# Performance work log

Hardware: AMD Instinct MI355X
Metric: run time of the kernel (lower is better)

## Reference

```python
import jax, jax.numpy as jnp
import numpy as np

N, E, DIN, DOUT = 10000, 160000, 256, 256
NEG_SLOPE = 0.2
BN_EPS = 1e-5
DROP_P = 0.5


def setup_inputs() -> dict:
    key = jax.random.key(0)
    ks = jax.random.split(key, 12)
    s = 1.0 / np.sqrt(DIN)
    return {
        "x": jax.random.normal(ks[0], (N, DIN), jnp.float32),
        "edge_index": jax.random.randint(ks[1], (2, E), 0, N, jnp.int64),
        "Wl": jax.random.normal(ks[2], (DIN, DOUT), jnp.float32) * s,
        "bl": jax.random.normal(ks[3], (DOUT,), jnp.float32) * s,
        "Wr": jax.random.normal(ks[4], (DIN, DOUT), jnp.float32) * s,
        "br": jax.random.normal(ks[5], (DOUT,), jnp.float32) * s,
        "att": jax.random.normal(ks[6], (DOUT,), jnp.float32) * (1.0 / np.sqrt(DOUT)),
        "bias": jax.random.normal(ks[7], (DOUT,), jnp.float32) * 0.01,
        "gamma": jnp.ones((DOUT,), jnp.float32),
        "beta": jnp.zeros((DOUT,), jnp.float32),
        "dropout_u": jax.random.uniform(ks[8], (N, DOUT), jnp.float32),
    }


def reference(x, edge_index, Wl, bl, Wr, br, att, bias, gamma, beta, dropout_u):
    n = x.shape[0]
    # GATv2Conv (heads=1): separate source/target linear maps
    xl = x @ Wl + bl  # source features [N, DOUT]
    xr = x @ Wr + br  # target features [N, DOUT]
    # add self-loops (PyG default add_self_loops=True)
    loop = jnp.arange(n, dtype=edge_index.dtype)
    src = jnp.concatenate([edge_index[0], loop])  # [E+N]
    dst = jnp.concatenate([edge_index[1], loop])
    # GATv2 attention: e = att . LeakyReLU(xl_j + xr_i)
    h = jax.nn.leaky_relu(xl[src] + xr[dst], NEG_SLOPE)  # [E+N, DOUT]
    alpha = h @ att  # [E+N]
    # segment softmax over destination nodes
    amax = jax.ops.segment_max(alpha, dst, num_segments=n)
    alpha = jnp.exp(alpha - amax[dst])
    denom = jax.ops.segment_sum(alpha, dst, num_segments=n)
    alpha = alpha / denom[dst]
    # scatter-add aggregate of weighted source features
    out = jax.ops.segment_sum(xl[src] * alpha[:, None], dst, num_segments=n)
    out = out + bias
    # ReLU -> dropout(p=0.5, training) -> BatchNorm (training stats)
    out = jax.nn.relu(out)
    mask = (dropout_u >= DROP_P).astype(out.dtype) / (1.0 - DROP_P)
    out = out * mask
    mean = out.mean(axis=0)
    var = out.var(axis=0)  # biased, as BatchNorm uses for normalization
    out = gamma * (out - mean) * jax.lax.rsqrt(var + BN_EPS) + beta
    return out
```

## Files before the change

kernel.cpp:

```cpp
#include <hip/hip_runtime.h>
#include <hip/hip_bf16.h>
#include <math.h>

#define D 256
#define CAP 128
#define NEG_SLOPE 0.2f
#define BN_EPS 1e-5f
#define NBKT 64

typedef __attribute__((ext_vector_type(8))) short bf16x8;
typedef __attribute__((ext_vector_type(8))) unsigned short ushort8;
typedef __attribute__((ext_vector_type(4))) float f32x4;

__device__ inline unsigned short f2bf(float f) {
    union { float f; unsigned u; } v; v.f = f;
    unsigned u = v.u;
    unsigned r = u + 0x7FFFu + ((u >> 16) & 1u);
    return (unsigned short)(r >> 16);
}
__device__ inline float bf2f(unsigned short u) {
    union { unsigned u; float f; } v; v.u = ((unsigned)u) << 16; return v.f;
}

__device__ __forceinline__ void gload16(const void* g, void* l) {
    __builtin_amdgcn_global_load_lds(
        (const __attribute__((address_space(1))) unsigned int*)g,
        (__attribute__((address_space(3))) unsigned int*)l,
        16, 0, 0);
}

__global__ void prep_kernel(const float* __restrict__ X,
                            const float* __restrict__ Wl, const float* __restrict__ Wr,
                            int* __restrict__ zero_base, int nzero, int nzb,
                            unsigned short* __restrict__ Bt,
                            unsigned short* __restrict__ Xbf, int N) {
    int b = blockIdx.x;
    if (b < nzb) {
        int idx = b * 256 + threadIdx.x;
        if (idx < nzero) zero_base[idx] = 0;
    } else if (b < nzb + 512) {
        int n = b - nzb;
        int k = threadIdx.x;
        const float* W = (n < 256) ? Wl : Wr;
        int nn = n & 255;
        int ks = k ^ ((n & 7) << 3);
        Bt[(size_t)n * 256 + ks] = f2bf(W[(size_t)k * 256 + nn]);
    } else {
        int idx = (b - nzb - 512) * 256 + threadIdx.x;
        int row = idx >> 5;
        int k0 = (idx & 31) * 8;
        int ks = k0 ^ ((row & 7) << 3);
        ushort8 v = {0, 0, 0, 0, 0, 0, 0, 0};
        if (row < N) {
            const float* src = X + (size_t)row * 256 + k0;
            float4 f0 = *(const float4*)(src);
            float4 f1 = *(const float4*)(src + 4);
            v[0] = f2bf(f0.x); v[1] = f2bf(f0.y);
            v[2] = f2bf(f0.z); v[3] = f2bf(f0.w);
            v[4] = f2bf(f1.x); v[5] = f2bf(f1.y);
            v[6] = f2bf(f1.z); v[7] = f2bf(f1.w);
        }
        *(ushort8*)(Xbf + (size_t)row * 256 + ks) = v;
    }
}

__global__ __launch_bounds__(256) void gemm_scatter_kernel(
    const unsigned short* __restrict__ Xbf, const unsigned short* __restrict__ Bt,
    const float* __restrict__ bl, const float* __restrict__ br,
    const int* __restrict__ ei, int* __restrict__ counts, int* __restrict__ ssrc,
    unsigned short* __restrict__ xlbf, float* __restrict__ xr,
    int M, int E, int N, int ngemm)
{
    if ((int)blockIdx.x >= ngemm) {
        int e = (blockIdx.x - ngemm) * 256 + threadIdx.x;
        if (e < E + N) {
            int src, dst;
            if (e < E) { src = ei[e]; dst = ei[E + e]; }
            else       { src = dst = e - E; }
            int pos = atomicAdd(&counts[dst], 1);
            if (pos < CAP) ssrc[dst * CAP + pos] = src;
        }
        return;
    }

    __shared__ __align__(16) unsigned short As[64 * 128];
    __shared__ __align__(16) unsigned short Bs[64 * 128];

    const int tid = threadIdx.x;
    const int wave = tid >> 6, lane = tid & 63;
    const int m_l = lane & 15, quad = lane >> 4;
    const int row0 = (blockIdx.x >> 3) * 64;
    const int n0 = (blockIdx.x & 7) * 64;
    const int sw = (m_l & 7) << 3;

    f32x4 acc[4] = {};

    for (int k0 = 0; k0 < 256; k0 += 128) {
        __syncthreads();
        #pragma unroll
        for (int i = 0; i < 4; i++) {
            int L = (tid + i * 256) * 16;
            int r = L >> 8;
            int cb = L & 255;
            gload16((const char*)Xbf + (size_t)(row0 + r) * 512 + (size_t)k0 * 2 + cb,
                    (char*)As + L);
            gload16((const char*)Bt + (size_t)(n0 + r) * 512 + (size_t)k0 * 2 + cb,
                    (char*)Bs + L);
        }
        __syncthreads();

        #pragma unroll
        for (int kk0 = 0; kk0 < 128; kk0 += 32) {
            int ka = (kk0 + quad * 8) ^ sw;
            bf16x8 a = *(const bf16x8*)&As[(wave * 16 + m_l) * 128 + ka];
            #pragma unroll
            for (int c = 0; c < 4; c++) {
                bf16x8 b = *(const bf16x8*)&Bs[(c * 16 + m_l) * 128 + ka];
                acc[c] = __builtin_amdgcn_mfma_f32_16x16x32_bf16(a, b, acc[c], 0, 0, 0);
            }
        }
    }

    const bool isl = (n0 < 256);
    #pragma unroll
    for (int c = 0; c < 4; c++) {
        int col = n0 + c * 16 + m_l;
        int cc = col & 255;
        float bv = isl ? bl[cc] : br[cc];
        #pragma unroll
        for (int r = 0; r < 4; r++) {
            int row = row0 + wave * 16 + quad * 4 + r;
            if (row < M) {
                float v = acc[c][r] + bv;
                if (isl) xlbf[(size_t)row * 256 + cc] = f2bf(v);
                else     xr[(size_t)row * 256 + cc] = v;
            }
        }
    }
}

__device__ inline float dot8leaky(const float* f, float4 bA, float4 bB,
                                  float4 aA, float4 aB) {
    float h, s = 0.f;
    h = f[0] + bA.x; h = (h > 0.f) ? h : NEG_SLOPE * h; s += h * aA.x;
    h = f[1] + bA.y; h = (h > 0.f) ? h : NEG_SLOPE * h; s += h * aA.y;
    h = f[2] + bA.z; h = (h > 0.f) ? h : NEG_SLOPE * h; s += h * aA.z;
    h = f[3] + bA.w; h = (h > 0.f) ? h : NEG_SLOPE * h; s += h * aA.w;
    h = f[4] + bB.x; h = (h > 0.f) ? h : NEG_SLOPE * h; s += h * aB.x;
    h = f[5] + bB.y; h = (h > 0.f) ? h : NEG_SLOPE * h; s += h * aB.y;
    h = f[6] + bB.z; h = (h > 0.f) ? h : NEG_SLOPE * h; s += h * aB.z;
    h = f[7] + bB.w; h = (h > 0.f) ? h : NEG_SLOPE * h; s += h * aB.w;
    return s;
}

__global__ __launch_bounds__(256) void node_kernel(
    const unsigned short* __restrict__ xlbf, const float* __restrict__ xr,
    const float* __restrict__ att, const float* __restrict__ bias,
    const float* __restrict__ du, const int* __restrict__ counts,
    const int* __restrict__ ssrc, float* __restrict__ out,
    float* __restrict__ bsum, float* __restrict__ bsq, int N)
{
    __shared__ float ls[4][256];

    const int wave = threadIdx.x >> 6, lane = threadIdx.x & 63;
    const int i = blockIdx.x * 4 + wave;
    const bool valid = (i < N);
    const int hl = lane & 31;
    const int sid = lane >> 5;

    int cnt = valid ? counts[i] : 0;
    if (cnt > CAP) cnt = CAP;
    const int start = i * CAP, end = start + cnt;

    int srcv = (lane < cnt) ? ssrc[start + lane] : 0;

    const float4 attA = ((const float4*)att)[hl * 2];
    const float4 attB = ((const float4*)att)[hl * 2 + 1];
    const float4 zf4 = {0.f, 0.f, 0.f, 0.f};
    const float4 bA = valid ? ((const float4*)(xr + (size_t)i * D))[hl * 2] : zf4;
    const float4 bB = valid ? ((const float4*)(xr + (size_t)i * D))[hl * 2 + 1] : zf4;

    float m = -INFINITY, lsum = 0.f;
    float acc[8] = {0.f, 0.f, 0.f, 0.f, 0.f, 0.f, 0.f, 0.f};
    const ushort8 z8 = {0, 0, 0, 0, 0, 0, 0, 0};
    const unsigned short* xb = xlbf + hl * 8;

    int e = start + sid;

    if (cnt <= 64) {
        ushort8 p0, p1, p2, p3;
        {
            int o = sid;
            int a0 = __shfl(srcv, o);
            int a1 = __shfl(srcv, o + 2);
            int a2 = __shfl(srcv, o + 4);
            int a3 = __shfl(srcv, o + 6);
            p0 = (e     < end) ? *(const ushort8*)(xb + (size_t)a0 * D) : z8;
            p1 = (e + 2 < end) ? *(const ushort8*)(xb + (size_t)a1 * D) : z8;
            p2 = (e + 4 < end) ? *(const ushort8*)(xb + (size_t)a2 * D) : z8;
            p3 = (e + 6 < end) ? *(const ushort8*)(xb + (size_t)a3 * D) : z8;
        }

        while (e < end) {
            ushort8 c0 = p0, c1 = p1, c2 = p2, c3 = p3;
            bool v1 = (e + 2 < end), v2 = (e + 4 < end), v3 = (e + 6 < end);
            int en = e + 8;
            {
                int on = en - start;
                int a0 = __shfl(srcv, on);
                int a1 = __shfl(srcv, on + 2);
                int a2 = __shfl(srcv, on + 4);
                int a3 = __shfl(srcv, on + 6);
                p0 = (en     < end) ? *(const ushort8*)(xb + (size_t)a0 * D) : z8;
                p1 = (en + 2 < end) ? *(const ushort8*)(xb + (size_t)a1 * D) : z8;
                p2 = (en + 4 < end) ? *(const ushort8*)(xb + (size_t)a2 * D) : z8;
                p3 = (en + 6 < end) ? *(const ushort8*)(xb + (size_t)a3 * D) : z8;
            }

            float f0[8], f1[8], f2[8], f3[8];
            #pragma unroll
            for (int k = 0; k < 8; k++) {
                f0[k] = bf2f(c0[k]); f1[k] = bf2f(c1[k]);
                f2[k] = bf2f(c2[k]); f3[k] = bf2f(c3[k]);
            }

            float s0 = dot8leaky(f0, bA, bB, attA, attB);
            float s1 = dot8leaky(f1, bA, bB, attA, attB);
            float s2 = dot8leaky(f2, bA, bB, attA, attB);
            float s3 = dot8leaky(f3, bA, bB, attA, attB);

            #pragma unroll
            for (int off = 1; off < 32; off <<= 1) {
                s0 += __shfl_xor(s0, off);
                s1 += __shfl_xor(s1, off);
                s2 += __shfl_xor(s2, off);
                s3 += __shfl_xor(s3, off);
            }
            if (!v1) s1 = -INFINITY;
            if (!v2) s2 = -INFINITY;
            if (!v3) s3 = -INFINITY;

            float mnew = fmaxf(fmaxf(m, fmaxf(s0, s1)), fmaxf(s2, s3));
            float sc = __expf(m - mnew);
            float e0e = __expf(s0 - mnew);
            float e1e = __expf(s1 - mnew);
            float e2e = __expf(s2 - mnew);
            float e3e = __expf(s3 - mnew);
            lsum = lsum * sc + e0e + e1e + e2e + e3e;
            #pragma unroll
            for (int k = 0; k < 8; k++) {
                acc[k] = acc[k] * sc + e0e * f0[k] + e1e * f1[k]
                                     + e2e * f2[k] + e3e * f3[k];
            }
            m = mnew;
            e = en;
        }
    } else {
        ushort8 p0, p1, p2, p3;
        p0 = (e     < end) ? *(const ushort8*)(xb + (size_t)ssrc[e]     * D) : z8;
        p1 = (e + 2 < end) ? *(const ushort8*)(xb + (size_t)ssrc[e + 2] * D) : z8;
        p2 = (e + 4 < end) ? *(const ushort8*)(xb + (size_t)ssrc[e + 4] * D) : z8;
        p3 = (e + 6 < end) ? *(const ushort8*)(xb + (size_t)ssrc[e + 6] * D) : z8;

        while (e < end) {
            ushort8 c0 = p0, c1 = p1, c2 = p2, c3 = p3;
            bool v1 = (e + 2 < end), v2 = (e + 4 < end), v3 = (e + 6 < end);
            int en = e + 8;
            p0 = (en     < end) ? *(const ushort8*)(xb + (size_t)ssrc[en]     * D) : z8;
            p1 = (en + 2 < end) ? *(const ushort8*)(xb + (size_t)ssrc[en + 2] * D) : z8;
            p2 = (en + 4 < end) ? *(const ushort8*)(xb + (size_t)ssrc[en + 4] * D) : z8;
            p3 = (en + 6 < end) ? *(const ushort8*)(xb + (size_t)ssrc[en + 6] * D) : z8;

            float f0[8], f1[8], f2[8], f3[8];
            #pragma unroll
            for (int k = 0; k < 8; k++) {
                f0[k] = bf2f(c0[k]); f1[k] = bf2f(c1[k]);
                f2[k] = bf2f(c2[k]); f3[k] = bf2f(c3[k]);
            }

            float s0 = dot8leaky(f0, bA, bB, attA, attB);
            float s1 = dot8leaky(f1, bA, bB, attA, attB);
            float s2 = dot8leaky(f2, bA, bB, attA, attB);
            float s3 = dot8leaky(f3, bA, bB, attA, attB);

            #pragma unroll
            for (int off = 1; off < 32; off <<= 1) {
                s0 += __shfl_xor(s0, off);
                s1 += __shfl_xor(s1, off);
                s2 += __shfl_xor(s2, off);
                s3 += __shfl_xor(s3, off);
            }
            if (!v1) s1 = -INFINITY;
            if (!v2) s2 = -INFINITY;
            if (!v3) s3 = -INFINITY;

            float mnew = fmaxf(fmaxf(m, fmaxf(s0, s1)), fmaxf(s2, s3));
            float sc = __expf(m - mnew);
            float e0e = __expf(s0 - mnew);
            float e1e = __expf(s1 - mnew);
            float e2e = __expf(s2 - mnew);
            float e3e = __expf(s3 - mnew);
            lsum = lsum * sc + e0e + e1e + e2e + e3e;
            #pragma unroll
            for (int k = 0; k < 8; k++) {
                acc[k] = acc[k] * sc + e0e * f0[k] + e1e * f1[k]
                                     + e2e * f2[k] + e3e * f3[k];
            }
            m = mnew;
            e = en;
        }
    }

    {
        float mO = __shfl_xor(m, 32);
        float lO = __shfl_xor(lsum, 32);
        float accO[8];
        #pragma unroll
        for (int k = 0; k < 8; k++) accO[k] = __shfl_xor(acc[k], 32);
        float mn = fmaxf(m, mO);
        float wS = (m  == -INFINITY) ? 0.f : __expf(m - mn);
        float wO = (mO == -INFINITY) ? 0.f : __expf(mO - mn);
        lsum = lsum * wS + lO * wO;
        #pragma unroll
        for (int k = 0; k < 8; k++) acc[k] = acc[k] * wS + accO[k] * wO;
    }

    float ov[8];
    if (lane < 32) {
        if (valid) {
            float inv = 1.f / lsum;
            float4 biA = ((const float4*)bias)[hl * 2];
            float4 biB = ((const float4*)bias)[hl * 2 + 1];
            float4 uA = ((const float4*)(du + (size_t)i * D))[hl * 2];
            float4 uB = ((const float4*)(du + (size_t)i * D))[hl * 2 + 1];
            float4 oA, oB;
            oA.x = fmaxf(acc[0] * inv + biA.x, 0.f); oA.x = (uA.x >= 0.5f) ? 2.f * oA.x : 0.f;
            oA.y = fmaxf(acc[1] * inv + biA.y, 0.f); oA.y = (uA.y >= 0.5f) ? 2.f * oA.y : 0.f;
            oA.z = fmaxf(acc[2] * inv + biA.z, 0.f); oA.z = (uA.z >= 0.5f) ? 2.f * oA.z : 0.f;
            oA.w = fmaxf(acc[3] * inv + biA.w, 0.f); oA.w = (uA.w >= 0.5f) ? 2.f * oA.w : 0.f;
            oB.x = fmaxf(acc[4] * inv + biB.x, 0.f); oB.x = (uB.x >= 0.5f) ? 2.f * oB.x : 0.f;
            oB.y = fmaxf(acc[5] * inv + biB.y, 0.f); oB.y = (uB.y >= 0.5f) ? 2.f * oB.y : 0.f;
            oB.z = fmaxf(acc[6] * inv + biB.z, 0.f); oB.z = (uB.z >= 0.5f) ? 2.f * oB.z : 0.f;
            oB.w = fmaxf(acc[7] * inv + biB.w, 0.f); oB.w = (uB.w >= 0.5f) ? 2.f * oB.w : 0.f;
            ((float4*)(out + (size_t)i * D))[hl * 2] = oA;
            ((float4*)(out + (size_t)i * D))[hl * 2 + 1] = oB;
            ov[0] = oA.x; ov[1] = oA.y; ov[2] = oA.z; ov[3] = oA.w;
            ov[4] = oB.x; ov[5] = oB.y; ov[6] = oB.z; ov[7] = oB.w;
        } else {
            #pragma unroll
            for (int k = 0; k < 8; k++) ov[k] = 0.f;
        }
        #pragma unroll
        for (int k = 0; k < 8; k++) ls[wave][hl * 8 + k] = ov[k];
    }
    __syncthreads();

    {
        int t = threadIdx.x;
        float s = 0.f, s2 = 0.f;
        #pragma unroll
        for (int w = 0; w < 4; w++) {
            float v = ls[w][t];
            s += v; s2 += v * v;
        }
        int bkt = (blockIdx.x & (NBKT - 1)) * 256 + t;
        atomicAdd(&bsum[bkt], s);
        atomicAdd(&bsq[bkt], s2);
    }
}

__global__ __launch_bounds__(256) void bn_apply_kernel(
    float* __restrict__ out,
    const float* __restrict__ bsum, const float* __restrict__ bsq,
    const float* __restrict__ gamma, const float* __restrict__ beta, int N)
{
    __shared__ float scaleL[256], shiftL[256];
    const int t = threadIdx.x;
    float s = 0.f, s2 = 0.f;
    #pragma unroll 8
    for (int b = 0; b < NBKT; b++) {
        s += bsum[b * 256 + t];
        s2 += bsq[b * 256 + t];
    }
    float invN = 1.f / (float)N;
    float mean = s * invN;
    float var = s2 * invN - mean * mean;
    float rs = rsqrtf(var + BN_EPS);
    float sc = gamma[t] * rs;
    scaleL[t] = sc;
    shiftL[t] = beta[t] - mean * sc;
    __syncthreads();

    const int c4 = t & 63;
    float4 scv, shv;
    scv.x = scaleL[c4 * 4];     shv.x = shiftL[c4 * 4];
    scv.y = scaleL[c4 * 4 + 1]; shv.y = shiftL[c4 * 4 + 1];
    scv.z = scaleL[c4 * 4 + 2]; shv.z = shiftL[c4 * 4 + 2];
    scv.w = scaleL[c4 * 4 + 3]; shv.w = shiftL[c4 * 4 + 3];

    for (int row = blockIdx.x * 4 + (t >> 6); row < N; row += gridDim.x * 4) {
        float4 v = ((float4*)(out + (size_t)row * D))[c4];
        v.x = v.x * scv.x + shv.x;
        v.y = v.y * scv.y + shv.y;
        v.z = v.z * scv.z + shv.z;
        v.w = v.w * scv.w + shv.w;
        ((float4*)(out + (size_t)row * D))[c4] = v;
    }
}

extern "C" void kernel_launch(void* const* d_in, const int* in_sizes, int n_in,
                              void* d_out, int out_size, void* d_ws, size_t ws_size,
                              hipStream_t stream) {
    const float* x     = (const float*)d_in[0];
    const int*   ei    = (const int*)d_in[1];
    const float* Wl    = (const float*)d_in[2];
    const float* bl    = (const float*)d_in[3];
    const float* Wr    = (const float*)d_in[4];
    const float* br    = (const float*)d_in[5];
    const float* att   = (const float*)d_in[6];
    const float* bias  = (const float*)d_in[7];
    const float* gamma = (const float*)d_in[8];
    const float* beta  = (const float*)d_in[9];
    const float* du    = (const float*)d_in[10];

    const int N = in_sizes[0] / D;
    const int E = in_sizes[1] / 2;
    const int Mpad = (N + 63) & ~63;

    int* ws = (int*)d_ws;
    size_t off = 0;
    float* xr       = (float*)(ws + off); off += (size_t)N * D;
    unsigned short* xlbf = (unsigned short*)(ws + off); off += (size_t)N * D / 2;
    unsigned short* Xbf  = (unsigned short*)(ws + off); off += (size_t)Mpad * D / 2;
    unsigned short* Bt   = (unsigned short*)(ws + off); off += 512 * 256 / 2;
    int*   ssrc     = ws + off;           off += (size_t)N * CAP;
    float* bsum     = (float*)(ws + off); off += NBKT * 256;
    float* bsq      = (float*)(ws + off); off += NBKT * 256;
    int*   counts   = ws + off;           off += N;
    int nzero = 2 * NBKT * 256 + N;
    int nzb = (nzero + 255) / 256;

    int nconv = (Mpad * 32) / 256;
    prep_kernel<<<nzb + 512 + nconv, 256, 0, stream>>>(
        x, Wl, Wr, (int*)bsum, nzero, nzb, Bt, Xbf, N);

    int nMtiles = (N + 63) / 64;
    int ngemm = nMtiles * 8;
    int nscat = (E + N + 255) / 256;
    gemm_scatter_kernel<<<ngemm + nscat, 256, 0, stream>>>(
        Xbf, Bt, bl, br, ei, counts, ssrc, xlbf, xr, N, E, N, ngemm);

    node_kernel<<<(N + 3) / 4, 256, 0, stream>>>(
        xlbf, xr, att, bias, du, counts, ssrc, (float*)d_out, bsum, bsq, N);

    bn_apply_kernel<<<256, 256, 0, stream>>>(
        (float*)d_out, bsum, bsq, gamma, beta, N);
}
```

Baseline: 143.3 us.

## Swizzle GEMM block order into 8x8 groups and hoist node-kernel loads early

The GEMM block index is remapped so that consecutive blocks cover 8x8 groups of (row tile, column tile) instead of walking all 8 column tiles of one row. This is meant to improve L2 reuse of the X and weight tiles, at the cost of padding the grid and some blocks returning early. In the node kernel, the ssrc load is made unconditional and the dropout-mask loads are issued at the start, so their latency overlaps the aggregation loop. This raises register pressure and reads unused ssrc slots, which are never used afterwards.

```diff
diff --git a/kernel.cpp b/kernel.cpp
--- a/kernel.cpp
+++ b/kernel.cpp
@@ -69,7 +69,7 @@
     const float* __restrict__ bl, const float* __restrict__ br,
     const int* __restrict__ ei, int* __restrict__ counts, int* __restrict__ ssrc,
     unsigned short* __restrict__ xlbf, float* __restrict__ xr,
-    int M, int E, int N, int ngemm)
+    int M, int E, int N, int ngemm, int nMtiles)
 {
     if ((int)blockIdx.x >= ngemm) {
         int e = (blockIdx.x - ngemm) * 256 + threadIdx.x;
@@ -83,14 +83,19 @@
         return;
     }
 
+    const int b = blockIdx.x;
+    const int r = (b & 7) + 8 * (b >> 6);
+    const int c = (b >> 3) & 7;
+    if (r >= nMtiles) return;
+
     __shared__ __align__(16) unsigned short As[64 * 128];
     __shared__ __align__(16) unsigned short Bs[64 * 128];
 
     const int tid = threadIdx.x;
     const int wave = tid >> 6, lane = tid & 63;
     const int m_l = lane & 15, quad = lane >> 4;
-    const int row0 = (blockIdx.x >> 3) * 64;
-    const int n0 = (blockIdx.x & 7) * 64;
+    const int row0 = r * 64;
+    const int n0 = c * 64;
     const int sw = (m_l & 7) << 3;
 
     f32x4 acc[4] = {};
@@ -100,11 +105,11 @@
         #pragma unroll
         for (int i = 0; i < 4; i++) {
             int L = (tid + i * 256) * 16;
-            int r = L >> 8;
+            int rr = L >> 8;
             int cb = L & 255;
-            gload16((const char*)Xbf + (size_t)(row0 + r) * 512 + (size_t)k0 * 2 + cb,
+            gload16((const char*)Xbf + (size_t)(row0 + rr) * 512 + (size_t)k0 * 2 + cb,
                     (char*)As + L);
-            gload16((const char*)Bt + (size_t)(n0 + r) * 512 + (size_t)k0 * 2 + cb,
+            gload16((const char*)Bt + (size_t)(n0 + rr) * 512 + (size_t)k0 * 2 + cb,
                     (char*)Bs + L);
         }
         __syncthreads();
@@ -114,26 +119,26 @@
             int ka = (kk0 + quad * 8) ^ sw;
             bf16x8 a = *(const bf16x8*)&As[(wave * 16 + m_l) * 128 + ka];
             #pragma unroll
-            for (int c = 0; c < 4; c++) {
-                bf16x8 b = *(const bf16x8*)&Bs[(c * 16 + m_l) * 128 + ka];
-                acc[c] = __builtin_amdgcn_mfma_f32_16x16x32_bf16(a, b, acc[c], 0, 0, 0);
+            for (int cc = 0; cc < 4; cc++) {
+                bf16x8 bv = *(const bf16x8*)&Bs[(cc * 16 + m_l) * 128 + ka];
+                acc[cc] = __builtin_amdgcn_mfma_f32_16x16x32_bf16(a, bv, acc[cc], 0, 0, 0);
             }
         }
     }
 
     const bool isl = (n0 < 256);
     #pragma unroll
-    for (int c = 0; c < 4; c++) {
-        int col = n0 + c * 16 + m_l;
-        int cc = col & 255;
-        float bv = isl ? bl[cc] : br[cc];
-        #pragma unroll
-        for (int r = 0; r < 4; r++) {
-            int row = row0 + wave * 16 + quad * 4 + r;
+    for (int cc = 0; cc < 4; cc++) {
+        int col = n0 + cc * 16 + m_l;
+        int col8 = col & 255;
+        float bv = isl ? bl[col8] : br[col8];
+        #pragma unroll
+        for (int rr = 0; rr < 4; rr++) {
+            int row = row0 + wave * 16 + quad * 4 + rr;
             if (row < M) {
-                float v = acc[c][r] + bv;
-                if (isl) xlbf[(size_t)row * 256 + cc] = f2bf(v);
-                else     xr[(size_t)row * 256 + cc] = v;
+                float v = acc[cc][rr] + bv;
+                if (isl) xlbf[(size_t)row * 256 + col8] = f2bf(v);
+                else     xr[(size_t)row * 256 + col8] = v;
             }
         }
     }
@@ -168,17 +173,24 @@
     const int hl = lane & 31;
     const int sid = lane >> 5;
 
+    const int start = i * CAP;
+
     int cnt = valid ? counts[i] : 0;
-    if (cnt > CAP) cnt = CAP;
-    const int start = i * CAP, end = start + cnt;
-
-    int srcv = (lane < cnt) ? ssrc[start + lane] : 0;
-
-    const float4 attA = ((const float4*)att)[hl * 2];
-    const float4 attB = ((const float4*)att)[hl * 2 + 1];
+    int srcv = valid ? ssrc[start + lane] : 0;
     const float4 zf4 = {0.f, 0.f, 0.f, 0.f};
     const float4 bA = valid ? ((const float4*)(xr + (size_t)i * D))[hl * 2] : zf4;
     const float4 bB = valid ? ((const float4*)(xr + (size_t)i * D))[hl * 2 + 1] : zf4;
+    float4 uA = zf4, uB = zf4;
+    if (valid && lane < 32) {
+        uA = ((const float4*)(du + (size_t)i * D))[hl * 2];
+        uB = ((const float4*)(du + (size_t)i * D))[hl * 2 + 1];
+    }
+
+    const float4 attA = ((const float4*)att)[hl * 2];
+    const float4 attB = ((const float4*)att)[hl * 2 + 1];
+
+    if (cnt > CAP) cnt = CAP;
+    const int end = start + cnt;
 
     float m = -INFINITY, lsum = 0.f;
     float acc[8] = {0.f, 0.f, 0.f, 0.f, 0.f, 0.f, 0.f, 0.f};
@@ -331,8 +343,6 @@
             float inv = 1.f / lsum;
             float4 biA = ((const float4*)bias)[hl * 2];
             float4 biB = ((const float4*)bias)[hl * 2 + 1];
-            float4 uA = ((const float4*)(du + (size_t)i * D))[hl * 2];
-            float4 uB = ((const float4*)(du + (size_t)i * D))[hl * 2 + 1];
             float4 oA, oB;
             oA.x = fmaxf(acc[0] * inv + biA.x, 0.f); oA.x = (uA.x >= 0.5f) ? 2.f * oA.x : 0.f;
             oA.y = fmaxf(acc[1] * inv + biA.y, 0.f); oA.y = (uA.y >= 0.5f) ? 2.f * oA.y : 0.f;
@@ -445,10 +455,11 @@
         x, Wl, Wr, (int*)bsum, nzero, nzb, Bt, Xbf, N);
 
     int nMtiles = (N + 63) / 64;
-    int ngemm = nMtiles * 8;
+    int nMgroups = (nMtiles + 7) / 8;
+    int ngemm = nMgroups * 64;
     int nscat = (E + N + 255) / 256;
     gemm_scatter_kernel<<<ngemm + nscat, 256, 0, stream>>>(
-        Xbf, Bt, bl, br, ei, counts, ssrc, xlbf, xr, N, E, N, ngemm);
+        Xbf, Bt, bl, br, ei, counts, ssrc, xlbf, xr, N, E, N, ngemm, nMtiles);
 
     node_kernel<<<(N + 3) / 4, 256, 0, stream>>>(
         xlbf, xr, att, bias, du, counts, ssrc, (float*)d_out, bsum, bsq, N);
```

After: 143.1 us. No clear change (-0.2%).
